# Optimization experiments

Hardware: AMD Instinct MI355X
Metric: run time of the kernel (lower is better)

The kernel has to match this reference:

```python
import jax, jax.numpy as jnp
import numpy as np

B, T, D, E, F = 4, 2048, 1024, 8, 1024

def setup_inputs() -> dict:
    key = jax.random.key(0)
    ks = jax.random.split(key, 5)
    s = lambda d: 1.0 / np.sqrt(d)
    return {
        "x": jax.random.normal(ks[0], (B, T, D), dtype=jnp.float32),
        "router_kernel_DE": jax.random.normal(ks[1], (D, E), dtype=jnp.float32) * s(D),
        "kernel_gating_EDF": jax.random.normal(ks[2], (E, D, F), dtype=jnp.float32) * s(D),
        "kernel_up_EDF": jax.random.normal(ks[3], (E, D, F), dtype=jnp.float32) * s(D),
        "kernel_down_EFD": jax.random.normal(ks[4], (E, F, D), dtype=jnp.float32) * s(F),
        "top_k": 2,
    }

def reference(x, router_kernel_DE, kernel_gating_EDF, kernel_up_EDF, kernel_down_EFD, top_k):
    # ---- Router ----
    router_logits_BTE = jnp.einsum('BTD,DE->BTE', x, router_kernel_DE)
    probs_BTE = jax.nn.softmax(router_logits_BTE.astype(jnp.float32), axis=-1)
    weights_BTX, selected_BTX = jax.lax.top_k(probs_BTE, top_k)
    # module re-normalizes top-k weights with a second softmax (faithful)
    norm_weights_BTX = jax.nn.softmax(weights_BTX, axis=-1)
    # ---- combine weights to dense per-expert weights ----
    one_hot_BTXE = jax.nn.one_hot(selected_BTX, num_classes=E, dtype=jnp.float32)
    full_weights_BTE = jnp.sum(one_hot_BTXE * norm_weights_BTX[..., None], axis=2)
    # ---- dense all-experts MLP (apply_expert_weight_before_computation=False) ----
    gating_BTEF = jnp.einsum('BTD,EDF->BTEF', x, kernel_gating_EDF)
    up_BTEF = jnp.einsum('BTD,EDF->BTEF', x, kernel_up_EDF)
    fuse_BTEF = jax.nn.silu(gating_BTEF) * up_BTEF
    down_BTED = jnp.einsum('BTEF,EFD->BTED', fuse_BTEF, kernel_down_EFD)
    out_BTD = jnp.einsum('BTED,BTE->BTD', down_BTED, full_weights_BTE)
    return out_BTD
```

## Files before the change

kernel.cpp:

```cpp
#include <hip/hip_runtime.h>
#include <hip/hip_bf16.h>
#include <math.h>

#define NTOK 8192
#define D_DIM 1024
#define E_DIM 8
#define F_DIM 1024

#define CNT_STRIDE 32

typedef __attribute__((ext_vector_type(8))) short bf16x8;
typedef __attribute__((ext_vector_type(4))) float f32x4;

typedef const __attribute__((address_space(1))) unsigned int* as1_uint_ptr;
typedef __attribute__((address_space(3))) unsigned int* as3_uint_ptr;

__device__ __forceinline__ void async_load16(const void* g, void* l) {
    __builtin_amdgcn_global_load_lds((as1_uint_ptr)g, (as3_uint_ptr)l, 16, 0, 0);
}

__device__ __forceinline__ float bf2f(unsigned short b) {
    unsigned int u = ((unsigned int)b) << 16;
    return __builtin_bit_cast(float, u);
}
__device__ __forceinline__ unsigned short f2bf(float f) {
    __hip_bfloat16 h = __float2bfloat16(f);
    return __builtin_bit_cast(unsigned short, h);
}


__global__ __launch_bounds__(512) void router_cast_kernel(
    const float* __restrict__ x,
    const float* __restrict__ Wr,
    int* __restrict__ cnt,
    int* __restrict__ tok_of,
    float* __restrict__ wt2,
    unsigned short* __restrict__ xb)
{
    __shared__ int lcnt[E_DIM];
    __shared__ int lbase[E_DIM];
    __shared__ int lbuf[E_DIM][64];

    const int tid = threadIdx.x;
    const int wv = tid >> 6;
    const int lane = tid & 63;
    if (tid < E_DIM) lcnt[tid] = 0;
    __syncthreads();

    #pragma unroll
    for (int it = 0; it < 4; ++it) {
        const int t = blockIdx.x * 32 + wv * 4 + it;
        const float* xrow = x + (size_t)t * D_DIM;
        unsigned short* xbrow = xb + (size_t)t * D_DIM;

        float p[E_DIM];
        #pragma unroll
        for (int e = 0; e < E_DIM; ++e) p[e] = 0.f;

        #pragma unroll
        for (int i = 0; i < 4; ++i) {
            const int d = i * 256 + lane * 4;
            float4 v = *(const float4*)(xrow + d);
            ushort4 o;
            o.x = f2bf(v.x); o.y = f2bf(v.y); o.z = f2bf(v.z); o.w = f2bf(v.w);
            *(ushort4*)(xbrow + d) = o;
            const float* wr = Wr + (size_t)d * E_DIM;
            float xv[4] = {v.x, v.y, v.z, v.w};
            #pragma unroll
            for (int q = 0; q < 4; ++q) {
                float4 w0 = *(const float4*)(wr + q * 8);
                float4 w1 = *(const float4*)(wr + q * 8 + 4);
                p[0] += xv[q] * w0.x; p[1] += xv[q] * w0.y;
                p[2] += xv[q] * w0.z; p[3] += xv[q] * w0.w;
                p[4] += xv[q] * w1.x; p[5] += xv[q] * w1.y;
                p[6] += xv[q] * w1.z; p[7] += xv[q] * w1.w;
            }
        }

        #pragma unroll
        for (int off = 32; off > 0; off >>= 1) {
            #pragma unroll
            for (int e = 0; e < E_DIM; ++e)
                p[e] += __shfl_xor(p[e], off, 64);
        }

        if (lane == 0) {
            float m = p[0];
            #pragma unroll
            for (int e = 1; e < E_DIM; ++e) m = fmaxf(m, p[e]);
            float pr[E_DIM], sum = 0.f;
            #pragma unroll
            for (int e = 0; e < E_DIM; ++e) { pr[e] = expf(p[e] - m); sum += pr[e]; }
            float inv = 1.f / sum;
            #pragma unroll
            for (int e = 0; e < E_DIM; ++e) pr[e] *= inv;
            int e0 = 0;
            #pragma unroll
            for (int e = 1; e < E_DIM; ++e) if (pr[e] > pr[e0]) e0 = e;
            int e1 = (e0 == 0) ? 1 : 0;
            #pragma unroll
            for (int e = 0; e < E_DIM; ++e) { if (e != e0 && pr[e] > pr[e1]) e1 = e; }
            float b = expf(pr[e1] - pr[e0]);
            float w0 = 1.f / (1.f + b);
            float w1 = b / (1.f + b);
            int p0 = atomicAdd(&lcnt[e0], 1);
            lbuf[e0][p0] = t * 2 + 0;
            int p1 = atomicAdd(&lcnt[e1], 1);
            lbuf[e1][p1] = t * 2 + 1;
            wt2[t * 2 + 0] = w0;
            wt2[t * 2 + 1] = w1;
        }
    }
    __syncthreads();
    if (tid < E_DIM) lbase[tid] = atomicAdd(&cnt[tid * CNT_STRIDE], lcnt[tid]);
    __syncthreads();
    #pragma unroll
    for (int e = 0; e < E_DIM; ++e) {
        int n = lcnt[e];
        if (tid < n) tok_of[e * NTOK + lbase[e] + tid] = lbuf[e][tid];
    }
}

__global__ __launch_bounds__(256) void transpose_cast_kernel(
    const float* __restrict__ Wg, const float* __restrict__ Wu,
    const float* __restrict__ Wd,
    unsigned short* __restrict__ WgT, unsigned short* __restrict__ WuT,
    unsigned short* __restrict__ WdT)
{
    const int m = blockIdx.z;
    const float* src;
    unsigned short* dst;
    if (m < 8)       { src = Wg + (size_t)m * 1048576;        dst = WgT + (size_t)m * 1048576; }
    else if (m < 16) { src = Wu + (size_t)(m - 8) * 1048576;  dst = WuT + (size_t)(m - 8) * 1048576; }
    else             { src = Wd + (size_t)(m - 16) * 1048576; dst = WdT + (size_t)(m - 16) * 1048576; }

    const int c0 = blockIdx.x * 64;
    const int r0 = blockIdx.y * 64;
    __shared__ float tile[64][65];
    const int tid = threadIdx.x;
    const int tr = tid >> 4;
    const int tc = (tid & 15) * 4;
    #pragma unroll
    for (int p = 0; p < 4; ++p) {
        float4 v = *(const float4*)(src + (size_t)(r0 + p * 16 + tr) * 1024 + c0 + tc);
        tile[p * 16 + tr][tc + 0] = v.x;
        tile[p * 16 + tr][tc + 1] = v.y;
        tile[p * 16 + tr][tc + 2] = v.z;
        tile[p * 16 + tr][tc + 3] = v.w;
    }
    __syncthreads();
    const int orow = tid >> 3;
    const int ocol = (tid & 7) * 8;
    #pragma unroll
    for (int p = 0; p < 2; ++p) {
        int fr = p * 32 + orow;
        union { unsigned short s[8]; uint4 v; } pk;
        #pragma unroll
        for (int q = 0; q < 8; ++q) pk.s[q] = f2bf(tile[ocol + q][fr]);
        *(uint4*)&dst[(size_t)(c0 + fr) * 1024 + r0 + ocol] = pk.v;
    }
}

__global__ __launch_bounds__(256, 2) void gateup_mfma(
    const unsigned short* __restrict__ xb,
    const unsigned short* __restrict__ WgT,
    const unsigned short* __restrict__ WuT,
    const int* __restrict__ cnt,
    const int* __restrict__ tok_of,
    unsigned short* __restrict__ H)
{
    const int e = blockIdx.y;
    const int rowTile = blockIdx.x >> 3;
    const int colTile = blockIdx.x & 7;
    const int rows = cnt[e * CNT_STRIDE];
    const int rowBase = rowTile * 128;
    if (rowBase >= rows) return;
    const int n0 = colTile * 128;

    __shared__ short As[128 * 32];
    __shared__ short Bg[128 * 32];
    __shared__ short Bu[128 * 32];
    __shared__ int toks[128];

    const int tid = threadIdx.x;
    if (tid < 128) {
        int idx = rowBase + tid;
        toks[tid] = tok_of[e * NTOK + (idx < rows ? idx : rows - 1)];
    }
    __syncthreads();

    const int lane = tid & 63;
    const int w = tid >> 6;
    const int seg0 = w * 2, seg1 = w * 2 + 1;
    const int sr = lane >> 2;
    const int swz = (sr >> 1) & 3;
    const int sk = ((lane & 3) ^ swz) * 8;

    const int ar0 = seg0 * 16 + sr;
    const int ar1 = seg1 * 16 + sr;
    const unsigned short* aG0 = xb + (size_t)(toks[ar0] >> 1) * D_DIM + sk;
    const unsigned short* aG1 = xb + (size_t)(toks[ar1] >> 1) * D_DIM + sk;
    const unsigned short* WgTe = WgT + (size_t)e * F_DIM * D_DIM;
    const unsigned short* WuTe = WuT + (size_t)e * F_DIM * D_DIM;
    const unsigned short* gG0 = WgTe + (size_t)(n0 + ar0) * D_DIM + sk;
    const unsigned short* gG1 = WgTe + (size_t)(n0 + ar1) * D_DIM + sk;
    const unsigned short* uG0 = WuTe + (size_t)(n0 + ar0) * D_DIM + sk;
    const unsigned short* uG1 = WuTe + (size_t)(n0 + ar1) * D_DIM + sk;

    short* aL0 = &As[seg0 * 512];
    short* aL1 = &As[seg1 * 512];
    short* gL0 = &Bg[seg0 * 512];
    short* gL1 = &Bg[seg1 * 512];
    short* uL0 = &Bu[seg0 * 512];
    short* uL1 = &Bu[seg1 * 512];

    const int mseg = (w >> 1) * 4;
    const int nseg = (w & 1) * 4;
    const int mbase = (w >> 1) * 64;
    const int nbase = (w & 1) * 64;
    const int fr = lane & 15;
    const int rd = (4 * fr + ((lane >> 4) ^ ((fr >> 1) & 3))) * 8;

    f32x4 accg[4][4], accu[4][4];
    #pragma unroll
    for (int i = 0; i < 4; ++i)
        #pragma unroll
        for (int j = 0; j < 4; ++j) { accg[i][j] = (f32x4)(0.f); accu[i][j] = (f32x4)(0.f); }

    for (int k0 = 0; k0 < D_DIM; k0 += 32) {
        async_load16(aG0 + k0, aL0);
        async_load16(aG1 + k0, aL1);
        async_load16(gG0 + k0, gL0);
        async_load16(gG1 + k0, gL1);
        async_load16(uG0 + k0, uL0);
        async_load16(uG1 + k0, uL1);
        __syncthreads();

        bf16x8 a[4], g[4], u[4];
        #pragma unroll
        for (int i = 0; i < 4; ++i)
            a[i] = *(const bf16x8*)&As[(mseg + i) * 512 + rd];
        #pragma unroll
        for (int j = 0; j < 4; ++j) {
            g[j] = *(const bf16x8*)&Bg[(nseg + j) * 512 + rd];
            u[j] = *(const bf16x8*)&Bu[(nseg + j) * 512 + rd];
        }
        #pragma unroll
        for (int i = 0; i < 4; ++i)
            #pragma unroll
            for (int j = 0; j < 4; ++j) {
                accg[i][j] = __builtin_amdgcn_mfma_f32_16x16x32_bf16(a[i], g[j], accg[i][j], 0, 0, 0);
                accu[i][j] = __builtin_amdgcn_mfma_f32_16x16x32_bf16(a[i], u[j], accu[i][j], 0, 0, 0);
            }
        __syncthreads();
    }

    const int erow = (lane >> 4) * 4;
    #pragma unroll
    for (int i = 0; i < 4; ++i) {
        #pragma unroll
        for (int r = 0; r < 4; ++r) {
            int row = mbase + i * 16 + erow + r;
            int idx = rowBase + row;
            if (idx < rows) {
                int tok2 = toks[row];
                unsigned short* hrow = H + (size_t)tok2 * F_DIM + n0 + nbase;
                #pragma unroll
                for (int j = 0; j < 4; ++j) {
                    float gg = accg[i][j][r];
                    float uu = accu[i][j][r];
                    float h = gg / (1.f + __expf(-gg)) * uu;
                    hrow[j * 16 + fr] = f2bf(h);
                }
            }
        }
    }
}

__global__ __launch_bounds__(256, 2) void down_mfma(
    const unsigned short* __restrict__ H,
    const unsigned short* __restrict__ WdT,
    const int* __restrict__ cnt,
    const int* __restrict__ tok_of,
    unsigned short* __restrict__ Hd)
{
    const int e = blockIdx.y;
    const int rowTile = blockIdx.x >> 3;
    const int colTile = blockIdx.x & 7;
    const int rows = cnt[e * CNT_STRIDE];
    const int rowBase = rowTile * 128;
    if (rowBase >= rows) return;
    const int n0 = colTile * 128;

    __shared__ short As[128 * 32];
    __shared__ short Bs[128 * 32];
    __shared__ int toks[128];

    const int tid = threadIdx.x;
    if (tid < 128) {
        int idx = rowBase + tid;
        toks[tid] = tok_of[e * NTOK + (idx < rows ? idx : rows - 1)];
    }
    __syncthreads();

    const int lane = tid & 63;
    const int w = tid >> 6;
    const int seg0 = w * 2, seg1 = w * 2 + 1;
    const int sr = lane >> 2;
    const int swz = (sr >> 1) & 3;
    const int sk = ((lane & 3) ^ swz) * 8;

    const int ar0 = seg0 * 16 + sr;
    const int ar1 = seg1 * 16 + sr;
    const unsigned short* aG0 = H + (size_t)toks[ar0] * F_DIM + sk;
    const unsigned short* aG1 = H + (size_t)toks[ar1] * F_DIM + sk;
    const unsigned short* WdTe = WdT + (size_t)e * D_DIM * F_DIM;
    const unsigned short* bG0 = WdTe + (size_t)(n0 + ar0) * F_DIM + sk;
    const unsigned short* bG1 = WdTe + (size_t)(n0 + ar1) * F_DIM + sk;

    short* aL0 = &As[seg0 * 512];
    short* aL1 = &As[seg1 * 512];
    short* bL0 = &Bs[seg0 * 512];
    short* bL1 = &Bs[seg1 * 512];

    const int mseg = (w >> 1) * 4;
    const int nseg = (w & 1) * 4;
    const int mbase = (w >> 1) * 64;
    const int nbase = (w & 1) * 64;
    const int fr = lane & 15;
    const int rd = (4 * fr + ((lane >> 4) ^ ((fr >> 1) & 3))) * 8;

    f32x4 acc[4][4];
    #pragma unroll
    for (int i = 0; i < 4; ++i)
        #pragma unroll
        for (int j = 0; j < 4; ++j) acc[i][j] = (f32x4)(0.f);

    for (int k0 = 0; k0 < F_DIM; k0 += 32) {
        async_load16(aG0 + k0, aL0);
        async_load16(aG1 + k0, aL1);
        async_load16(bG0 + k0, bL0);
        async_load16(bG1 + k0, bL1);
        __syncthreads();

        bf16x8 a[4], b[4];
        #pragma unroll
        for (int i = 0; i < 4; ++i)
            a[i] = *(const bf16x8*)&As[(mseg + i) * 512 + rd];
        #pragma unroll
        for (int j = 0; j < 4; ++j)
            b[j] = *(const bf16x8*)&Bs[(nseg + j) * 512 + rd];
        #pragma unroll
        for (int i = 0; i < 4; ++i)
            #pragma unroll
            for (int j = 0; j < 4; ++j)
                acc[i][j] = __builtin_amdgcn_mfma_f32_16x16x32_bf16(a[i], b[j], acc[i][j], 0, 0, 0);
        __syncthreads();
    }

    const int erow = (lane >> 4) * 4;
    #pragma unroll
    for (int i = 0; i < 4; ++i) {
        #pragma unroll
        for (int r = 0; r < 4; ++r) {
            int row = mbase + i * 16 + erow + r;
            int idx = rowBase + row;
            if (idx < rows) {
                int tok2 = toks[row];
                unsigned short* orow = Hd + (size_t)tok2 * D_DIM + n0 + nbase;
                #pragma unroll
                for (int j = 0; j < 4; ++j)
                    orow[j * 16 + fr] = f2bf(acc[i][j][r]);
            }
        }
    }
}

__global__ __launch_bounds__(256) void combine_kernel(
    const unsigned short* __restrict__ Hd,
    const float* __restrict__ wt2,
    float* __restrict__ out)
{
    const int t = blockIdx.x;
    const int tid = threadIdx.x;
    const float w0 = wt2[2 * t];
    const float w1 = wt2[2 * t + 1];
    const int c = tid * 4;
    ushort4 a = *(const ushort4*)&Hd[(size_t)(2 * t) * D_DIM + c];
    ushort4 b = *(const ushort4*)&Hd[(size_t)(2 * t + 1) * D_DIM + c];
    float4 o;
    o.x = w0 * bf2f(a.x) + w1 * bf2f(b.x);
    o.y = w0 * bf2f(a.y) + w1 * bf2f(b.y);
    o.z = w0 * bf2f(a.z) + w1 * bf2f(b.z);
    o.w = w0 * bf2f(a.w) + w1 * bf2f(b.w);
    *(float4*)(out + (size_t)t * D_DIM + c) = o;
}

extern "C" void kernel_launch(void* const* d_in, const int* in_sizes, int n_in,
                              void* d_out, int out_size, void* d_ws, size_t ws_size,
                              hipStream_t stream) {
    const float* x  = (const float*)d_in[0];
    const float* Wr = (const float*)d_in[1];
    const float* Wg = (const float*)d_in[2];
    const float* Wu = (const float*)d_in[3];
    const float* Wd = (const float*)d_in[4];
    float* out = (float*)d_out;

    char* ws = (char*)d_ws;
    int*   cnt    = (int*)ws;
    int*   tok_of = (int*)(ws + 1024);
    float* wt2    = (float*)(ws + 1024 + E_DIM * NTOK * 4);
    char*  base   = ws + (1 << 20);
    unsigned short* xb  = (unsigned short*)(base);
    unsigned short* Hd  = (unsigned short*)(base);
    unsigned short* WgT = (unsigned short*)(base + (16ll << 20));
    unsigned short* WuT = (unsigned short*)(base + (32ll << 20));
    unsigned short* WdT = (unsigned short*)(base + (48ll << 20));
    unsigned short* H   = (unsigned short*)(base + (64ll << 20));

    hipMemsetAsync(cnt, 0, E_DIM * CNT_STRIDE * sizeof(int), stream);

    router_cast_kernel<<<NTOK / 32, 512, 0, stream>>>(x, Wr, cnt, tok_of, wt2, xb);
    transpose_cast_kernel<<<dim3(16, 16, 24), 256, 0, stream>>>(Wg, Wu, Wd, WgT, WuT, WdT);

    gateup_mfma<<<dim3((NTOK / 128) * (F_DIM / 128), E_DIM), 256, 0, stream>>>(
        xb, WgT, WuT, cnt, tok_of, H);
    down_mfma<<<dim3((NTOK / 128) * (D_DIM / 128), E_DIM), 256, 0, stream>>>(
        H, WdT, cnt, tok_of, Hd);
    combine_kernel<<<NTOK, 256, 0, stream>>>(Hd, wt2, out);
}
```

Measured before the change: 372.9 us.

## Double-buffer MFMA K-loops and fuse weighted combine into down GEMM via atomics

Both expert GEMMs now use two LDS buffers: the next K-slice is prefetched with async global-to-LDS loads while the current slice feeds MFMAs, and explicit vmcnt waits plus raw barriers replace __syncthreads. The separate combine kernel is removed. The down GEMM scales its rows by the routing weight and atomically adds fp32 results into a zeroed output, which drops the bf16 Hd round trip and one launch. Launch bounds are raised to 3 blocks per CU. The trade-off is doubled LDS use, a possible register squeeze from the larger occupancy target, and float atomic contention plus nondeterministic summation order.

```diff
diff --git a/kernel.cpp b/kernel.cpp
--- a/kernel.cpp
+++ b/kernel.cpp
@@ -27,6 +27,11 @@
     __hip_bfloat16 h = __float2bfloat16(f);
     return __builtin_bit_cast(unsigned short, h);
 }
+
+#define WAIT_VM6() __builtin_amdgcn_s_waitcnt(0xF76)
+#define WAIT_VM4() __builtin_amdgcn_s_waitcnt(0xF74)
+#define WAIT_VM0() __builtin_amdgcn_s_waitcnt(0xF70)
+#define CLOBBER()  asm volatile("" ::: "memory")
 
 
 __global__ __launch_bounds__(512) void router_cast_kernel(
@@ -161,7 +166,7 @@
     }
 }
 
-__global__ __launch_bounds__(256, 2) void gateup_mfma(
+__global__ __launch_bounds__(256, 3) void gateup_mfma(
     const unsigned short* __restrict__ xb,
     const unsigned short* __restrict__ WgT,
     const unsigned short* __restrict__ WuT,
@@ -177,9 +182,9 @@
     if (rowBase >= rows) return;
     const int n0 = colTile * 128;
 
-    __shared__ short As[128 * 32];
-    __shared__ short Bg[128 * 32];
-    __shared__ short Bu[128 * 32];
+    __shared__ short As[2 * 4096];
+    __shared__ short Bg[2 * 4096];
+    __shared__ short Bu[2 * 4096];
     __shared__ int toks[128];
 
     const int tid = threadIdx.x;
@@ -207,13 +212,6 @@
     const unsigned short* uG0 = WuTe + (size_t)(n0 + ar0) * D_DIM + sk;
     const unsigned short* uG1 = WuTe + (size_t)(n0 + ar1) * D_DIM + sk;
 
-    short* aL0 = &As[seg0 * 512];
-    short* aL1 = &As[seg1 * 512];
-    short* gL0 = &Bg[seg0 * 512];
-    short* gL1 = &Bg[seg1 * 512];
-    short* uL0 = &Bu[seg0 * 512];
-    short* uL1 = &Bu[seg1 * 512];
-
     const int mseg = (w >> 1) * 4;
     const int nseg = (w & 1) * 4;
     const int mbase = (w >> 1) * 64;
@@ -227,23 +225,38 @@
         #pragma unroll
         for (int j = 0; j < 4; ++j) { accg[i][j] = (f32x4)(0.f); accu[i][j] = (f32x4)(0.f); }
 
-    for (int k0 = 0; k0 < D_DIM; k0 += 32) {
-        async_load16(aG0 + k0, aL0);
-        async_load16(aG1 + k0, aL1);
-        async_load16(gG0 + k0, gL0);
-        async_load16(gG1 + k0, gL1);
-        async_load16(uG0 + k0, uL0);
-        async_load16(uG1 + k0, uL1);
-        __syncthreads();
+#define STAGE_GU(k0, poff) do {                                  \
+        async_load16(aG0 + (k0), &As[(poff) + seg0 * 512]);      \
+        async_load16(aG1 + (k0), &As[(poff) + seg1 * 512]);      \
+        async_load16(gG0 + (k0), &Bg[(poff) + seg0 * 512]);      \
+        async_load16(gG1 + (k0), &Bg[(poff) + seg1 * 512]);      \
+        async_load16(uG0 + (k0), &Bu[(poff) + seg0 * 512]);      \
+        async_load16(uG1 + (k0), &Bu[(poff) + seg1 * 512]);      \
+    } while (0)
+
+    STAGE_GU(0, 0);
+    int p = 0;
+    for (int it = 0; it < D_DIM / 32; ++it) {
+        const int poff = p << 12;
+        if (it < D_DIM / 32 - 1) {
+            STAGE_GU((it + 1) * 32, (p ^ 1) << 12);
+            CLOBBER();
+            WAIT_VM6();
+        } else {
+            CLOBBER();
+            WAIT_VM0();
+        }
+        __builtin_amdgcn_s_barrier();
+        CLOBBER();
 
         bf16x8 a[4], g[4], u[4];
         #pragma unroll
         for (int i = 0; i < 4; ++i)
-            a[i] = *(const bf16x8*)&As[(mseg + i) * 512 + rd];
+            a[i] = *(const bf16x8*)&As[poff + (mseg + i) * 512 + rd];
         #pragma unroll
         for (int j = 0; j < 4; ++j) {
-            g[j] = *(const bf16x8*)&Bg[(nseg + j) * 512 + rd];
-            u[j] = *(const bf16x8*)&Bu[(nseg + j) * 512 + rd];
+            g[j] = *(const bf16x8*)&Bg[poff + (nseg + j) * 512 + rd];
+            u[j] = *(const bf16x8*)&Bu[poff + (nseg + j) * 512 + rd];
         }
         #pragma unroll
         for (int i = 0; i < 4; ++i)
@@ -252,8 +265,12 @@
                 accg[i][j] = __builtin_amdgcn_mfma_f32_16x16x32_bf16(a[i], g[j], accg[i][j], 0, 0, 0);
                 accu[i][j] = __builtin_amdgcn_mfma_f32_16x16x32_bf16(a[i], u[j], accu[i][j], 0, 0, 0);
             }
-        __syncthreads();
-    }
+
+        CLOBBER();
+        __builtin_amdgcn_s_barrier();
+        p ^= 1;
+    }
+#undef STAGE_GU
 
     const int erow = (lane >> 4) * 4;
     #pragma unroll
@@ -277,12 +294,13 @@
     }
 }
 
-__global__ __launch_bounds__(256, 2) void down_mfma(
+__global__ __launch_bounds__(256, 3) void down_mfma(
     const unsigned short* __restrict__ H,
     const unsigned short* __restrict__ WdT,
     const int* __restrict__ cnt,
     const int* __restrict__ tok_of,
-    unsigned short* __restrict__ Hd)
+    const float* __restrict__ wt2,
+    float* __restrict__ out)
 {
     const int e = blockIdx.y;
     const int rowTile = blockIdx.x >> 3;
@@ -292,14 +310,17 @@
     if (rowBase >= rows) return;
     const int n0 = colTile * 128;
 
-    __shared__ short As[128 * 32];
-    __shared__ short Bs[128 * 32];
+    __shared__ short As[2 * 4096];
+    __shared__ short Bs[2 * 4096];
     __shared__ int toks[128];
+    __shared__ float wts[128];
 
     const int tid = threadIdx.x;
     if (tid < 128) {
         int idx = rowBase + tid;
-        toks[tid] = tok_of[e * NTOK + (idx < rows ? idx : rows - 1)];
+        int tok = tok_of[e * NTOK + (idx < rows ? idx : rows - 1)];
+        toks[tid] = tok;
+        wts[tid] = wt2[tok];
     }
     __syncthreads();
 
@@ -318,11 +339,6 @@
     const unsigned short* bG0 = WdTe + (size_t)(n0 + ar0) * F_DIM + sk;
     const unsigned short* bG1 = WdTe + (size_t)(n0 + ar1) * F_DIM + sk;
 
-    short* aL0 = &As[seg0 * 512];
-    short* aL1 = &As[seg1 * 512];
-    short* bL0 = &Bs[seg0 * 512];
-    short* bL1 = &Bs[seg1 * 512];
-
     const int mseg = (w >> 1) * 4;
     const int nseg = (w & 1) * 4;
     const int mbase = (w >> 1) * 64;
@@ -336,27 +352,46 @@
         #pragma unroll
         for (int j = 0; j < 4; ++j) acc[i][j] = (f32x4)(0.f);
 
-    for (int k0 = 0; k0 < F_DIM; k0 += 32) {
-        async_load16(aG0 + k0, aL0);
-        async_load16(aG1 + k0, aL1);
-        async_load16(bG0 + k0, bL0);
-        async_load16(bG1 + k0, bL1);
-        __syncthreads();
+#define STAGE_D(k0, poff) do {                                   \
+        async_load16(aG0 + (k0), &As[(poff) + seg0 * 512]);      \
+        async_load16(aG1 + (k0), &As[(poff) + seg1 * 512]);      \
+        async_load16(bG0 + (k0), &Bs[(poff) + seg0 * 512]);      \
+        async_load16(bG1 + (k0), &Bs[(poff) + seg1 * 512]);      \
+    } while (0)
+
+    STAGE_D(0, 0);
+    int p = 0;
+    for (int it = 0; it < F_DIM / 32; ++it) {
+        const int poff = p << 12;
+        if (it < F_DIM / 32 - 1) {
+            STAGE_D((it + 1) * 32, (p ^ 1) << 12);
+            CLOBBER();
+            WAIT_VM4();
+        } else {
+            CLOBBER();
+            WAIT_VM0();
+        }
+        __builtin_amdgcn_s_barrier();
+        CLOBBER();
 
         bf16x8 a[4], b[4];
         #pragma unroll
         for (int i = 0; i < 4; ++i)
-            a[i] = *(const bf16x8*)&As[(mseg + i) * 512 + rd];
+            a[i] = *(const bf16x8*)&As[poff + (mseg + i) * 512 + rd];
         #pragma unroll
         for (int j = 0; j < 4; ++j)
-            b[j] = *(const bf16x8*)&Bs[(nseg + j) * 512 + rd];
+            b[j] = *(const bf16x8*)&Bs[poff + (nseg + j) * 512 + rd];
         #pragma unroll
         for (int i = 0; i < 4; ++i)
             #pragma unroll
             for (int j = 0; j < 4; ++j)
                 acc[i][j] = __builtin_amdgcn_mfma_f32_16x16x32_bf16(a[i], b[j], acc[i][j], 0, 0, 0);
-        __syncthreads();
-    }
+
+        CLOBBER();
+        __builtin_amdgcn_s_barrier();
+        p ^= 1;
+    }
+#undef STAGE_D
 
     const int erow = (lane >> 4) * 4;
     #pragma unroll
@@ -367,33 +402,14 @@
             int idx = rowBase + row;
             if (idx < rows) {
                 int tok2 = toks[row];
-                unsigned short* orow = Hd + (size_t)tok2 * D_DIM + n0 + nbase;
+                float wgt = wts[row];
+                float* orow = out + (size_t)(tok2 >> 1) * D_DIM + n0 + nbase;
                 #pragma unroll
                 for (int j = 0; j < 4; ++j)
-                    orow[j * 16 + fr] = f2bf(acc[i][j][r]);
+                    unsafeAtomicAdd(&orow[j * 16 + fr], wgt * acc[i][j][r]);
             }
         }
     }
-}
-
-__global__ __launch_bounds__(256) void combine_kernel(
-    const unsigned short* __restrict__ Hd,
-    const float* __restrict__ wt2,
-    float* __restrict__ out)
-{
-    const int t = blockIdx.x;
-    const int tid = threadIdx.x;
-    const float w0 = wt2[2 * t];
-    const float w1 = wt2[2 * t + 1];
-    const int c = tid * 4;
-    ushort4 a = *(const ushort4*)&Hd[(size_t)(2 * t) * D_DIM + c];
-    ushort4 b = *(const ushort4*)&Hd[(size_t)(2 * t + 1) * D_DIM + c];
-    float4 o;
-    o.x = w0 * bf2f(a.x) + w1 * bf2f(b.x);
-    o.y = w0 * bf2f(a.y) + w1 * bf2f(b.y);
-    o.z = w0 * bf2f(a.z) + w1 * bf2f(b.z);
-    o.w = w0 * bf2f(a.w) + w1 * bf2f(b.w);
-    *(float4*)(out + (size_t)t * D_DIM + c) = o;
 }
 
 extern "C" void kernel_launch(void* const* d_in, const int* in_sizes, int n_in,
@@ -412,13 +428,13 @@
     float* wt2    = (float*)(ws + 1024 + E_DIM * NTOK * 4);
     char*  base   = ws + (1 << 20);
     unsigned short* xb  = (unsigned short*)(base);
-    unsigned short* Hd  = (unsigned short*)(base);
     unsigned short* WgT = (unsigned short*)(base + (16ll << 20));
     unsigned short* WuT = (unsigned short*)(base + (32ll << 20));
     unsigned short* WdT = (unsigned short*)(base + (48ll << 20));
     unsigned short* H   = (unsigned short*)(base + (64ll << 20));
 
     hipMemsetAsync(cnt, 0, E_DIM * CNT_STRIDE * sizeof(int), stream);
+    hipMemsetAsync(d_out, 0, (size_t)out_size * sizeof(float), stream);
 
     router_cast_kernel<<<NTOK / 32, 512, 0, stream>>>(x, Wr, cnt, tok_of, wt2, xb);
     transpose_cast_kernel<<<dim3(16, 16, 24), 256, 0, stream>>>(Wg, Wu, Wd, WgT, WuT, WdT);
@@ -426,6 +442,5 @@
     gateup_mfma<<<dim3((NTOK / 128) * (F_DIM / 128), E_DIM), 256, 0, stream>>>(
         xb, WgT, WuT, cnt, tok_of, H);
     down_mfma<<<dim3((NTOK / 128) * (D_DIM / 128), E_DIM), 256, 0, stream>>>(
-        H, WdT, cnt, tok_of, Hd);
-    combine_kernel<<<NTOK, 256, 0, stream>>>(Hd, wt2, out);
-}
+        H, WdT, cnt, tok_of, wt2, out);
+}
```

After: 494.9 us. +32.7%, slower.
